# Performance work log

Hardware: AMD Instinct MI355X
Metric: run time of the kernel (lower is better)

The kernel has to match this reference:

```python
import jax, jax.numpy as jnp
import numpy as np

N, E, ET = 50000, 400000, 50000
F, ED, H, L = 64, 32, 128, 2


def _forward(x, edge_attr, target_edge_attr, node_W, node_b, edge_W, edge_b,
             pre_W, pre_b, post_W, post_b, lin_W, lin_b, bn_g, bn_b,
             em1_W, em1_b, em2_W, em2_b, edge_index):
    n = x.shape[0]
    h = node_W.shape[1]
    src, dst = edge_index[0], edge_index[1]
    x = x @ node_W + node_b                      # [N,H]
    ea = edge_attr @ edge_W + edge_b             # [E,H]
    tea = target_edge_attr @ edge_W + edge_b     # [Et,H]

    ones = jnp.ones((src.shape[0],), jnp.float32)
    cnt = jax.ops.segment_sum(ones, dst, num_segments=n)        # in-degree per node
    avg_deg_log = jnp.mean(jnp.log(cnt + 1.0))                  # PyG avg_deg['log'] from deg histogram
    deg = jnp.clip(cnt, 1.0)[:, None]
    amp = jnp.log(deg + 1.0) / avg_deg_log                      # 'amplification' scaler
    att = avg_deg_log / jnp.log(deg + 1.0)                      # 'attenuation' scaler
    cnt_c = jnp.clip(cnt, 1.0)[:, None]
    has = (cnt > 0)[:, None]

    nlayers = pre_W.shape[0]
    for i in range(nlayers):
        # pre-MLP on message cat([x_i(dst), x_j(src), edge_attr]); split matmul avoids [E,3H] concat
        Wd, Ws, We = pre_W[i, :h], pre_W[i, h:2 * h], pre_W[i, 2 * h:]
        m = x[dst] @ Wd + x[src] @ Ws + ea @ We + pre_b[i]      # [E,H]
        s = jax.ops.segment_sum(m, dst, num_segments=n)
        mean = s / cnt_c
        mean2 = jax.ops.segment_sum(m * m, dst, num_segments=n) / cnt_c
        std = jnp.sqrt(jax.nn.relu(mean2 - mean * mean) + 1e-5)  # PyG StdAggregation
        mn = jnp.where(has, jax.ops.segment_min(m, dst, num_segments=n), 0.0)
        mx = jnp.where(has, jax.ops.segment_max(m, dst, num_segments=n), 0.0)
        agg = jnp.concatenate([mean, mn, mx, std], axis=-1)     # [N,4H] aggregator order
        scaled = jnp.concatenate([agg, agg * amp, agg * att], axis=-1)  # [N,12H] scaler order
        # post-MLP on cat([x, scaled]); split matmul
        out = x @ post_W[i, :h] + scaled @ post_W[i, h:] + post_b[i]
        out = out @ lin_W[i] + lin_b[i]
        # BatchNorm (training mode, biased var, eps=1e-5)
        mu = out.mean(axis=0)
        var = jnp.mean((out - mu) ** 2, axis=0)
        bn = bn_g[i] * (out - mu) / jnp.sqrt(var + 1e-5) + bn_b[i]
        x = (x + jax.nn.relu(bn)) / 2
        # edge update: ea + MLP(cat([x[src], x[dst], ea])) / 2
        W1s, W1d, W1e = em1_W[i, :h], em1_W[i, h:2 * h], em1_W[i, 2 * h:]
        hid = jax.nn.relu(x[src] @ W1s + x[dst] @ W1d + ea @ W1e + em1_b[i])
        ea = ea + (hid @ em2_W[i] + em2_b[i]) / 2
    return (x, ea, tea)


def setup_inputs() -> dict:
    key = jax.random.key(0)
    ks = jax.random.split(key, 24)

    def w(k, shape):
        fan_in = shape[-2]
        return (jax.random.normal(k, shape, jnp.float32) / np.sqrt(fan_in)).astype(jnp.float32)

    inp = {
        'x': jax.random.normal(ks[0], (N, F), jnp.float32),
        'edge_attr': jax.random.normal(ks[1], (E, ED), jnp.float32),
        'target_edge_attr': jax.random.normal(ks[2], (ET, ED), jnp.float32),
        'node_W': w(ks[3], (F, H)), 'node_b': jnp.zeros((H,), jnp.float32),
        'edge_W': w(ks[4], (ED, H)), 'edge_b': jnp.zeros((H,), jnp.float32),
        'pre_W': w(ks[5], (L, 3 * H, H)), 'pre_b': jnp.zeros((L, H), jnp.float32),
        'post_W': w(ks[6], (L, 13 * H, H)), 'post_b': jnp.zeros((L, H), jnp.float32),
        'lin_W': w(ks[7], (L, H, H)), 'lin_b': jnp.zeros((L, H), jnp.float32),
        'bn_g': jnp.ones((L, H), jnp.float32), 'bn_b': jnp.zeros((L, H), jnp.float32),
        'em1_W': w(ks[8], (L, 3 * H, H)), 'em1_b': jnp.zeros((L, H), jnp.float32),
        'em2_W': w(ks[9], (L, H, H)), 'em2_b': jnp.zeros((L, H), jnp.float32),
        'edge_index': jax.random.randint(ks[10], (2, E), 0, N, dtype=jnp.int32),
    }
    return inp


def reference(x, edge_attr, target_edge_attr, node_W, node_b, edge_W, edge_b,
              pre_W, pre_b, post_W, post_b, lin_W, lin_b, bn_g, bn_b,
              em1_W, em1_b, em2_W, em2_b, edge_index):
    return _forward(x, edge_attr, target_edge_attr, node_W, node_b, edge_W, edge_b,
                    pre_W, pre_b, post_W, post_b, lin_W, lin_b, bn_g, bn_b,
                    em1_W, em1_b, em2_W, em2_b, edge_index)
```

## Files before the change

### kernel.cpp

```cpp
#include <hip/hip_runtime.h>
#include <math.h>

#define NN  50000
#define NE  400000
#define NTE 50000
#define FIN 64
#define EDIM 32
#define HD  128
#define NL  2
#define SCAN_B ((NN + 255) / 256)

typedef __attribute__((ext_vector_type(8))) short bf16x8;
typedef __attribute__((ext_vector_type(4))) short bf16x4;
typedef __attribute__((ext_vector_type(4))) float f32x4;

static __device__ __forceinline__ unsigned short f2bf(float f) {
    unsigned u = __float_as_uint(f);
    unsigned r = (u + 0x7fffu + ((u >> 16) & 1u)) >> 16;
    return (unsigned short)r;
}
static __device__ __forceinline__ float bfhi2f(unsigned u) { return __uint_as_float(u & 0xffff0000u); }
static __device__ __forceinline__ float bflo2f(unsigned u) { return __uint_as_float(u << 16); }

static __device__ __forceinline__ bf16x8 load_a8(const float* p, bool ok) {
    bf16x8 a = {};
    if (ok) {
        const float4 v0 = *(const float4*)(p);
        const float4 v1 = *(const float4*)(p + 4);
        a[0] = (short)f2bf(v0.x); a[1] = (short)f2bf(v0.y);
        a[2] = (short)f2bf(v0.z); a[3] = (short)f2bf(v0.w);
        a[4] = (short)f2bf(v1.x); a[5] = (short)f2bf(v1.y);
        a[6] = (short)f2bf(v1.z); a[7] = (short)f2bf(v1.w);
    }
    return a;
}
static __device__ __forceinline__ bf16x4 pack4(float4 a) {
    bf16x4 v;
    v[0]=(short)f2bf(a.x); v[1]=(short)f2bf(a.y); v[2]=(short)f2bf(a.z); v[3]=(short)f2bf(a.w);
    return v;
}

__global__ void __launch_bounds__(256) k_packW(const float* __restrict__ W,
        unsigned short* __restrict__ out, int K)
{
    const int tid = blockIdx.x * 256 + threadIdx.x;
    const int total = (K / 32) * 512;
    if (tid >= total) return;
    const int lane = tid & 63, nt = (tid >> 6) & 7, kb = tid >> 9;
    const int k0 = kb * 32 + (lane >> 4) * 8;
    const int col = nt * 16 + (lane & 15);
    bf16x8 v;
    #pragma unroll
    for (int j = 0; j < 8; ++j)
        v[j] = (short)f2bf(W[(size_t)(k0 + j) * HD + col]);
    *(bf16x8*)(out + (size_t)tid * 8) = v;
}

__global__ void __launch_bounds__(256) k_foldW(const float* __restrict__ edgeW,
        const float* __restrict__ edgeb, const float* __restrict__ We0,
        float* __restrict__ Wf, float* __restrict__ bf)
{
    const int tid = blockIdx.x * 256 + threadIdx.x;
    if (tid < 4096) {
        const int k = tid >> 7, c = tid & 127;
        float s = 0.f;
        for (int j = 0; j < 128; ++j) s += edgeW[k * HD + j] * We0[(size_t)j * HD + c];
        Wf[tid] = s;
    } else if (tid < 4224) {
        const int c = tid - 4096;
        float s = 0.f;
        for (int j = 0; j < 128; ++j) s += edgeb[j] * We0[(size_t)j * HD + c];
        bf[c] = s;
    }
}

template<int KB>
__global__ void __launch_bounds__(256) k_gemm_T(const float* A,
        const unsigned short* __restrict__ Wpk, const float* __restrict__ bias,
        float* C, int M)
{
    const int t = threadIdx.x, w = t >> 6, l = t & 63;
    const int n = blockIdx.x * 64 + w * 16 + (l & 15);
    const bool ok = n < M;
    const int q = l >> 4;
    const int K = KB * 32;
    f32x4 acc[8] = {};
    #pragma unroll
    for (int kb = 0; kb < KB; ++kb) {
        const bf16x8 b = load_a8(A + (size_t)n * K + kb * 32 + q * 8, ok);
        #pragma unroll
        for (int nt = 0; nt < 8; ++nt) {
            const bf16x8 aW = *(const bf16x8*)(Wpk + (((size_t)(kb * 8 + nt) * 64 + l) << 3));
            acc[nt] = __builtin_amdgcn_mfma_f32_16x16x32_bf16(aW, b, acc[nt], 0, 0, 0);
        }
    }
    if (ok) {
        float* pc = C + (size_t)n * HD + q * 4;
        #pragma unroll
        for (int nt = 0; nt < 8; ++nt) {
            const int col = nt * 16 + q * 4;
            float4 bv = bias ? *(const float4*)(bias + col) : make_float4(0.f,0.f,0.f,0.f);
            float4 o;
            o.x = acc[nt][0] + bv.x; o.y = acc[nt][1] + bv.y;
            o.z = acc[nt][2] + bv.z; o.w = acc[nt][3] + bv.w;
            *(float4*)(pc + nt * 16) = o;
        }
    }
}

template<int KB>
__global__ void __launch_bounds__(256) k_gemm2_Tb(const float* A,
        const unsigned short* __restrict__ W0, const unsigned short* __restrict__ W1,
        const float* __restrict__ b0, unsigned short* C0, unsigned short* C1, int M)
{
    const int t = threadIdx.x, w = t >> 6, l = t & 63;
    const int n = blockIdx.x * 64 + w * 16 + (l & 15);
    const bool ok = n < M;
    const int q = l >> 4;
    const int K = KB * 32;
    f32x4 a0[8] = {}, a1[8] = {};
    #pragma unroll
    for (int kb = 0; kb < KB; ++kb) {
        const bf16x8 b = load_a8(A + (size_t)n * K + kb * 32 + q * 8, ok);
        #pragma unroll
        for (int nt = 0; nt < 8; ++nt) {
            const bf16x8 u = *(const bf16x8*)(W0 + (((size_t)(kb * 8 + nt) * 64 + l) << 3));
            const bf16x8 v = *(const bf16x8*)(W1 + (((size_t)(kb * 8 + nt) * 64 + l) << 3));
            a0[nt] = __builtin_amdgcn_mfma_f32_16x16x32_bf16(u, b, a0[nt], 0, 0, 0);
            a1[nt] = __builtin_amdgcn_mfma_f32_16x16x32_bf16(v, b, a1[nt], 0, 0, 0);
        }
    }
    if (ok) {
        unsigned short* p0 = C0 + (size_t)n * HD + q * 4;
        unsigned short* p1 = C1 + (size_t)n * HD + q * 4;
        #pragma unroll
        for (int nt = 0; nt < 8; ++nt) {
            const int col = nt * 16 + q * 4;
            float4 bv = b0 ? *(const float4*)(b0 + col) : make_float4(0.f,0.f,0.f,0.f);
            float4 o0, o1;
            o0.x = a0[nt][0] + bv.x; o0.y = a0[nt][1] + bv.y;
            o0.z = a0[nt][2] + bv.z; o0.w = a0[nt][3] + bv.w;
            o1.x = a1[nt][0]; o1.y = a1[nt][1]; o1.z = a1[nt][2]; o1.w = a1[nt][3];
            *(bf16x4*)(p0 + nt * 16) = pack4(o0);
            *(bf16x4*)(p1 + nt * 16) = pack4(o1);
        }
    }
}

__global__ void __launch_bounds__(256) k_count(const int* __restrict__ d, int* __restrict__ cnt, int E)
{
    const int e = blockIdx.x * 256 + threadIdx.x;
    if (e < E) atomicAdd(&cnt[d[e]], 1);
}

__global__ void __launch_bounds__(256) k_avglog(const int* __restrict__ cnt, float* __restrict__ stats)
{
    float s = 0.f;
    for (int n = blockIdx.x * 256 + threadIdx.x; n < NN; n += gridDim.x * 256)
        s += logf((float)cnt[n] + 1.f);
    #pragma unroll
    for (int off = 32; off > 0; off >>= 1) s += __shfl_down(s, off);
    __shared__ float ls[4];
    if ((threadIdx.x & 63) == 0) ls[threadIdx.x >> 6] = s;
    __syncthreads();
    if (threadIdx.x == 0) unsafeAtomicAdd(stats, ls[0] + ls[1] + ls[2] + ls[3]);
}

__global__ void __launch_bounds__(256) k_scan_block(const int* __restrict__ cnt,
        int* __restrict__ incl, int* __restrict__ part)
{
    __shared__ int s[256];
    const int t = threadIdx.x;
    const int i = blockIdx.x * 256 + t;
    const int v = (i < NN) ? cnt[i] : 0;
    s[t] = v;
    __syncthreads();
    #pragma unroll
    for (int off = 1; off < 256; off <<= 1) {
        const int x = (t >= off) ? s[t - off] : 0;
        __syncthreads();
        s[t] += x;
        __syncthreads();
    }
    if (i < NN) incl[i] = s[t];
    if (t == 255) part[blockIdx.x] = s[255];
}

__global__ void __launch_bounds__(256) k_scan_part(const int* __restrict__ part,
        int* __restrict__ poff, int np)
{
    __shared__ int s[256];
    const int t = threadIdx.x;
    const int v = (t < np) ? part[t] : 0;
    s[t] = v;
    __syncthreads();
    #pragma unroll
    for (int off = 1; off < 256; off <<= 1) {
        const int x = (t >= off) ? s[t - off] : 0;
        __syncthreads();
        s[t] += x;
        __syncthreads();
    }
    poff[t] = s[t] - v;
}

__global__ void __launch_bounds__(256) k_scan_add(const int* __restrict__ incl,
        const int* __restrict__ cnt, const int* __restrict__ poff,
        int* __restrict__ row_start, int* __restrict__ cursor)
{
    const int i = blockIdx.x * 256 + threadIdx.x;
    if (i < NN) {
        const int excl = incl[i] - cnt[i] + poff[blockIdx.x];
        row_start[i] = excl;
        cursor[i] = excl;
    }
    if (i == 0) row_start[NN] = NE;
}

__global__ void __launch_bounds__(256) k_scatter(const int* __restrict__ dstp,
        int* cursor, int* __restrict__ sppos)
{
    const int e = blockIdx.x * 256 + threadIdx.x;
    if (e < NE) sppos[e] = atomicAdd(&cursor[dstp[e]], 1);
}

template<int KB>
__global__ void __launch_bounds__(256) k_msg_T(const float* __restrict__ EA,
        const unsigned short* __restrict__ Wpk, const float* __restrict__ bias,
        const unsigned short* __restrict__ xsb, const int* __restrict__ srcp,
        const int* __restrict__ sppos, unsigned short* __restrict__ mbuf)
{
    const int t = threadIdx.x, w = t >> 6, l = t & 63;
    const int e = blockIdx.x * 64 + w * 16 + (l & 15);
    const int q = l >> 4;
    f32x4 acc[8] = {};
    #pragma unroll
    for (int kb = 0; kb < KB; ++kb) {
        const bf16x8 bea = load_a8(EA + (size_t)e * (KB * 32) + kb * 32 + q * 8, true);
        #pragma unroll
        for (int nt = 0; nt < 8; ++nt) {
            const bf16x8 aW = *(const bf16x8*)(Wpk + (((size_t)(kb * 8 + nt) * 64 + l) << 3));
            acc[nt] = __builtin_amdgcn_mfma_f32_16x16x32_bf16(aW, bea, acc[nt], 0, 0, 0);
        }
    }
    const int sn = srcp[e], sp = sppos[e];
    const unsigned short* ps = xsb + (size_t)sn * HD + q * 4;
    unsigned short* pm = mbuf + (size_t)sp * HD + q * 4;
    #pragma unroll
    for (int nt = 0; nt < 8; ++nt) {
        const uint2 su = *(const uint2*)(ps + nt * 16);
        float4 o;
        o.x = acc[nt][0] + bflo2f(su.x); o.y = acc[nt][1] + bfhi2f(su.x);
        o.z = acc[nt][2] + bflo2f(su.y); o.w = acc[nt][3] + bfhi2f(su.y);
        if (bias) {
            const float4 bv = *(const float4*)(bias + nt * 16 + q * 4);
            o.x += bv.x; o.y += bv.y; o.z += bv.z; o.w += bv.w;
        }
        *(bf16x4*)(pm + nt * 16) = pack4(o);
    }
}

__global__ void __launch_bounds__(256) k_agg(const unsigned short* __restrict__ mbuf,
        const int* __restrict__ rs, const unsigned short* __restrict__ xdb,
        const float* __restrict__ stats, unsigned short* __restrict__ aggb)
{
    const int n = blockIdx.x * 4 + (threadIdx.x >> 6);
    if (n >= NN) return;
    const int lane = threadIdx.x & 63;
    const int c = lane * 2;
    const int s = rs[n], e = rs[n + 1];
    const unsigned xu = *(const unsigned*)(xdb + (size_t)n * HD + c);
    const float xv0 = bflo2f(xu), xv1 = bfhi2f(xu);
    float s0=0.f, s1=0.f, q0=0.f, q1=0.f;
    float mn0=INFINITY, mn1=INFINITY, mx0=-INFINITY, mx1=-INFINITY;
    for (int i = s; i < e; ++i) {
        const unsigned u = *(const unsigned*)(mbuf + (size_t)i * HD + c);
        const float v0 = bflo2f(u), v1 = bfhi2f(u);
        s0 += v0; s1 += v1;
        q0 += v0 * v0; q1 += v1 * v1;
        mn0 = fminf(mn0, v0); mn1 = fminf(mn1, v1);
        mx0 = fmaxf(mx0, v0); mx1 = fmaxf(mx1, v1);
    }
    const int deg = e - s;
    const float inv = 1.f / (float)(deg > 1 ? deg : 1);
    const float fd = (float)deg * inv;
    const float m0p = s0 * inv, m1p = s1 * inv;
    const float sd0 = sqrtf(fmaxf(q0 * inv - m0p * m0p, 0.f) + 1e-5f);
    const float sd1 = sqrtf(fmaxf(q1 * inv - m1p * m1p, 0.f) + 1e-5f);
    const bool has = deg > 0;
    const float v0[4] = { m0p + fd * xv0, has ? mn0 + xv0 : 0.f,
                          has ? mx0 + xv0 : 0.f, sd0 };
    const float v1[4] = { m1p + fd * xv1, has ? mn1 + xv1 : 0.f,
                          has ? mx1 + xv1 : 0.f, sd1 };
    const float avg = stats[0] * (1.f / (float)NN);
    const float lg = logf(fmaxf((float)deg, 1.f) + 1.f);
    const float amp = lg / avg, att = avg / lg;
    unsigned* a = (unsigned*)(aggb + (size_t)n * 1536 + c);
    #pragma unroll
    for (int sct = 0; sct < 4; ++sct) {
        a[sct * 64]       = (unsigned)f2bf(v0[sct])       | ((unsigned)f2bf(v1[sct]) << 16);
        a[256 + sct * 64] = (unsigned)f2bf(v0[sct] * amp) | ((unsigned)f2bf(v1[sct] * amp) << 16);
        a[512 + sct * 64] = (unsigned)f2bf(v0[sct] * att) | ((unsigned)f2bf(v1[sct] * att) << 16);
    }
}

__global__ void __launch_bounds__(256) k_post_lin_T(const float* __restrict__ x,
        const unsigned short* __restrict__ aggb, const unsigned short* __restrict__ PWpk,
        const float* __restrict__ pb, const unsigned short* __restrict__ LNpk,
        const float* __restrict__ lb, float* __restrict__ outb, int M)
{
    __shared__ unsigned short s_o16[64 * 128];
    const int t = threadIdx.x, w = t >> 6, l = t & 63;
    const int el = w * 16 + (l & 15);
    const int n = blockIdx.x * 64 + el;
    const bool ok = n < M;
    const int q = l >> 4;
    f32x4 acc[8] = {};
    #pragma unroll
    for (int kb = 0; kb < 4; ++kb) {
        const bf16x8 b = load_a8(x + (size_t)n * HD + kb * 32 + q * 8, ok);
        #pragma unroll
        for (int nt = 0; nt < 8; ++nt) {
            const bf16x8 aW = *(const bf16x8*)(PWpk + (((size_t)(kb * 8 + nt) * 64 + l) << 3));
            acc[nt] = __builtin_amdgcn_mfma_f32_16x16x32_bf16(aW, b, acc[nt], 0, 0, 0);
        }
    }
    const unsigned short* arow = aggb + (size_t)n * 1536 + q * 8;
    #pragma unroll 4
    for (int kb = 4; kb < 52; ++kb) {
        bf16x8 b = {};
        if (ok) b = *(const bf16x8*)(arow + (size_t)(kb - 4) * 32);
        #pragma unroll
        for (int nt = 0; nt < 8; ++nt) {
            const bf16x8 aW = *(const bf16x8*)(PWpk + (((size_t)(kb * 8 + nt) * 64 + l) << 3));
            acc[nt] = __builtin_amdgcn_mfma_f32_16x16x32_bf16(aW, b, acc[nt], 0, 0, 0);
        }
    }
    #pragma unroll
    for (int nt = 0; nt < 8; ++nt) {
        const int col = nt * 16 + q * 4;
        const float4 bv = *(const float4*)(pb + col);
        float4 o;
        o.x = acc[nt][0] + bv.x; o.y = acc[nt][1] + bv.y;
        o.z = acc[nt][2] + bv.z; o.w = acc[nt][3] + bv.w;
        const int bcol = nt * 32 + q * 8;
        const int slot = bcol >> 4;
        const int ba = el * 256 + ((slot ^ (el & 7)) << 4) + (bcol & 15);
        *(bf16x4*)((char*)s_o16 + ba) = pack4(o);
    }
    __syncthreads();
    f32x4 acc2[8] = {};
    #pragma unroll
    for (int kb = 0; kb < 4; ++kb) {
        const int slot = kb * 4 + q;
        const int ba = el * 256 + ((slot ^ (el & 7)) << 4);
        const bf16x8 bh = *(const bf16x8*)((const char*)s_o16 + ba);
        #pragma unroll
        for (int nt = 0; nt < 8; ++nt) {
            const bf16x8 aW = *(const bf16x8*)(LNpk + (((size_t)(kb * 8 + nt) * 64 + l) << 3));
            acc2[nt] = __builtin_amdgcn_mfma_f32_16x16x32_bf16(aW, bh, acc2[nt], 0, 0, 0);
        }
    }
    if (ok) {
        float* pc = outb + (size_t)n * HD + q * 4;
        #pragma unroll
        for (int nt = 0; nt < 8; ++nt) {
            const int col = nt * 16 + q * 4;
            const float4 bv = *(const float4*)(lb + col);
            float4 o;
            o.x = acc2[nt][0] + bv.x; o.y = acc2[nt][1] + bv.y;
            o.z = acc2[nt][2] + bv.z; o.w = acc2[nt][3] + bv.w;
            *(float4*)(pc + nt * 16) = o;
        }
    }
}

__global__ void __launch_bounds__(256) k_bnstats(const float* __restrict__ ob,
        float* __restrict__ bs, float* __restrict__ bq, int M)
{
    const int c = threadIdx.x & 127;
    const int gsub = threadIdx.x >> 7;
    float s = 0.f, qq = 0.f;
    for (int rr = blockIdx.x * 2 + gsub; rr < M; rr += gridDim.x * 2) {
        const float v = ob[(size_t)rr * HD + c];
        s += v; qq += v * v;
    }
    __shared__ float ls[2][HD], lq[2][HD];
    ls[gsub][c] = s; lq[gsub][c] = qq;
    __syncthreads();
    if (gsub == 0) {
        unsafeAtomicAdd(&bs[c], ls[0][c] + ls[1][c]);
        unsafeAtomicAdd(&bq[c], lq[0][c] + lq[1][c]);
    }
}

__global__ void __launch_bounds__(256) k_xupdate(float* x, const float* __restrict__ ob,
        const float* __restrict__ bs, const float* __restrict__ bq,
        const float* __restrict__ g, const float* __restrict__ bb)
{
    const int i = blockIdx.x * 256 + threadIdx.x;
    const int c0 = (i & 31) * 4;
    const float4 ov = ((const float4*)ob)[i];
    const float4 xv = ((const float4*)x)[i];
    const float o[4]  = {ov.x, ov.y, ov.z, ov.w};
    const float xo[4] = {xv.x, xv.y, xv.z, xv.w};
    float res[4];
    #pragma unroll
    for (int j = 0; j < 4; ++j) {
        const int c = c0 + j;
        const float mu  = bs[c] * (1.f / (float)NN);
        const float var = bq[c] * (1.f / (float)NN) - mu * mu;
        const float bn  = g[c] * (o[j] - mu) * rsqrtf(var + 1e-5f) + bb[c];
        res[j] = (xo[j] + fmaxf(bn, 0.f)) * 0.5f;
    }
    ((float4*)x)[i] = make_float4(res[0], res[1], res[2], res[3]);
}

__global__ void __launch_bounds__(256) k_edge_upd_T(float* ea,
        const unsigned short* __restrict__ W1epk, const unsigned short* __restrict__ e2pk,
        const float* __restrict__ e2b, const unsigned short* __restrict__ xs1b,
        const unsigned short* __restrict__ xd1b, const int* __restrict__ srcp,
        const int* __restrict__ dstp)
{
    __shared__ unsigned short s_hid[64 * 128];
    __shared__ float s_b2[128];
    const int t = threadIdx.x, w = t >> 6, l = t & 63;
    const int row0b = blockIdx.x * 64;
    if (t < 128) s_b2[t] = e2b[t];
    const int el = w * 16 + (l & 15);
    const int e = row0b + el;
    const int q = l >> 4, kq = q * 8;
    f32x4 acc1[8] = {};
    #pragma unroll
    for (int kb = 0; kb < 4; ++kb) {
        const bf16x8 bea = load_a8(ea + (size_t)e * HD + kb * 32 + kq, true);
        #pragma unroll
        for (int nt = 0; nt < 8; ++nt) {
            const bf16x8 aW = *(const bf16x8*)(W1epk + (((size_t)(kb * 8 + nt) * 64 + l) << 3));
            acc1[nt] = __builtin_amdgcn_mfma_f32_16x16x32_bf16(aW, bea, acc1[nt], 0, 0, 0);
        }
    }
    {
        const int sn = srcp[e], dn = dstp[e];
        const unsigned short* ps = xs1b + (size_t)sn * HD + q * 4;
        const unsigned short* pd = xd1b + (size_t)dn * HD + q * 4;
        #pragma unroll
        for (int nt = 0; nt < 8; ++nt) {
            const uint2 su = *(const uint2*)(ps + nt * 16);
            const uint2 du = *(const uint2*)(pd + nt * 16);
            float4 h;
            h.x = fmaxf(acc1[nt][0] + bflo2f(su.x) + bflo2f(du.x), 0.f);
            h.y = fmaxf(acc1[nt][1] + bfhi2f(su.x) + bfhi2f(du.x), 0.f);
            h.z = fmaxf(acc1[nt][2] + bflo2f(su.y) + bflo2f(du.y), 0.f);
            h.w = fmaxf(acc1[nt][3] + bfhi2f(su.y) + bfhi2f(du.y), 0.f);
            const int bcol = nt * 32 + q * 8;
            const int slot = bcol >> 4;
            const int ba = el * 256 + ((slot ^ (el & 7)) << 4) + (bcol & 15);
            *(bf16x4*)((char*)s_hid + ba) = pack4(h);
        }
    }
    __syncthreads();
    f32x4 acc2[8] = {};
    #pragma unroll
    for (int kb = 0; kb < 4; ++kb) {
        const int slot = kb * 4 + q;
        const int ba = el * 256 + ((slot ^ (el & 7)) << 4);
        const bf16x8 bh = *(const bf16x8*)((const char*)s_hid + ba);
        #pragma unroll
        for (int nt = 0; nt < 8; ++nt) {
            const bf16x8 aW = *(const bf16x8*)(e2pk + (((size_t)(kb * 8 + nt) * 64 + l) << 3));
            acc2[nt] = __builtin_amdgcn_mfma_f32_16x16x32_bf16(aW, bh, acc2[nt], 0, 0, 0);
        }
    }
    {
        float* pe = ea + (size_t)e * HD + q * 4;
        #pragma unroll
        for (int nt = 0; nt < 8; ++nt) {
            const float4 eo = *(const float4*)(pe + nt * 16);
            const float4 bv = *(const float4*)(&s_b2[nt * 16 + q * 4]);
            float4 o;
            o.x = eo.x + (acc2[nt][0] + bv.x) * 0.5f;
            o.y = eo.y + (acc2[nt][1] + bv.y) * 0.5f;
            o.z = eo.z + (acc2[nt][2] + bv.z) * 0.5f;
            o.w = eo.w + (acc2[nt][3] + bv.w) * 0.5f;
            *(float4*)(pe + nt * 16) = o;
        }
    }
}

extern "C" void kernel_launch(void* const* d_in, const int* in_sizes, int n_in,
                              void* d_out, int out_size, void* d_ws, size_t ws_size,
                              hipStream_t stream)
{
    const float* x0    = (const float*)d_in[0];
    const float* eatr  = (const float*)d_in[1];
    const float* teatr = (const float*)d_in[2];
    const float* nodeW = (const float*)d_in[3];
    const float* nodeb = (const float*)d_in[4];
    const float* edgeW = (const float*)d_in[5];
    const float* edgeb = (const float*)d_in[6];
    const float* preW  = (const float*)d_in[7];
    const float* preb  = (const float*)d_in[8];
    const float* postW = (const float*)d_in[9];
    const float* postb = (const float*)d_in[10];
    const float* linW  = (const float*)d_in[11];
    const float* linb  = (const float*)d_in[12];
    const float* bng   = (const float*)d_in[13];
    const float* bnb   = (const float*)d_in[14];
    const float* em1W  = (const float*)d_in[15];
    const float* em1b  = (const float*)d_in[16];
    const float* em2W  = (const float*)d_in[17];
    const float* em2b  = (const float*)d_in[18];
    const int*   eidx  = (const int*)d_in[19];
    const int* srcp = eidx;
    const int* dstp = eidx + NE;

    float* out_x  = (float*)d_out;
    float* out_ea = out_x + (size_t)NN * HD;
    float* out_te = out_ea + (size_t)NE * HD;

    const size_t NH = (size_t)NN * HD;
    const size_t EH = (size_t)NE * HD;
    unsigned short* xdb = (unsigned short*)d_ws;
    unsigned short* xsb = xdb + NH;
    float* outb  = (float*)(xsb + NH);
    float* stats = outb + NH;
    float* Wf    = stats + 512;
    float* bfold = Wf + 4096;
    int*   cnt      = (int*)(bfold + 128);
    int*   row_start = cnt + NN;
    int*   cursor   = row_start + NN + 1;
    int*   tmpincl  = cursor + NN;
    int*   part     = tmpincl + NN;
    int*   poff     = part + 256;
    int*   sppos    = poff + 256;
    unsigned short* mbuf = (unsigned short*)(((uintptr_t)(sppos + NE) + 15) & ~(uintptr_t)15);
    unsigned short* aggb = mbuf + EH;
    unsigned short* pk   = aggb + (size_t)NN * 1536;
    const size_t KBSZ = 512 * 8;
    unsigned short* pkPost = pk;
    unsigned short* pkPre  = pkPost + 104 * KBSZ;
    unsigned short* pkEm1  = pkPre  + 24 * KBSZ;
    unsigned short* pkLin  = pkEm1  + 24 * KBSZ;
    unsigned short* pkEm2  = pkLin  + 8 * KBSZ;
    unsigned short* pkNode = pkEm2  + 8 * KBSZ;
    unsigned short* pkEdge = pkNode + 2 * KBSZ;
    unsigned short* pkWe0f = pkEdge + 1 * KBSZ;

    hipMemsetAsync(cnt, 0, NN * sizeof(int), stream);
    hipMemsetAsync(stats, 0, 512 * sizeof(float), stream);

    k_packW<<<208, 256, 0, stream>>>(postW, pkPost, 3328);
    k_packW<<<48, 256, 0, stream>>>(preW,  pkPre,  768);
    k_packW<<<48, 256, 0, stream>>>(em1W,  pkEm1,  768);
    k_packW<<<16, 256, 0, stream>>>(linW,  pkLin,  256);
    k_packW<<<16, 256, 0, stream>>>(em2W,  pkEm2,  256);
    k_packW<<<4, 256, 0, stream>>>(nodeW, pkNode, 64);
    k_packW<<<2, 256, 0, stream>>>(edgeW, pkEdge, 32);
    k_foldW<<<17, 256, 0, stream>>>(edgeW, edgeb, preW + 256 * HD, Wf, bfold);
    k_packW<<<2, 256, 0, stream>>>(Wf, pkWe0f, 32);

    k_gemm_T<1><<<(NE + 63) / 64, 256, 0, stream>>>(eatr, pkEdge, edgeb, out_ea, NE);
    k_gemm_T<1><<<(NTE + 63) / 64, 256, 0, stream>>>(teatr, pkEdge, edgeb, out_te, NTE);
    k_gemm_T<2><<<(NN + 63) / 64, 256, 0, stream>>>(x0, pkNode, nodeb, out_x, NN);

    k_count<<<(NE + 255) / 256, 256, 0, stream>>>(dstp, cnt, NE);
    k_avglog<<<256, 256, 0, stream>>>(cnt, stats);
    k_scan_block<<<SCAN_B, 256, 0, stream>>>(cnt, tmpincl, part);
    k_scan_part<<<1, 256, 0, stream>>>(part, poff, SCAN_B);
    k_scan_add<<<SCAN_B, 256, 0, stream>>>(tmpincl, cnt, poff, row_start, cursor);
    k_scatter<<<(NE + 255) / 256, 256, 0, stream>>>(dstp, cursor, sppos);

    const int gn = (NN + 63) / 64;
    const int ge = NE / 64;

    for (int l = 0; l < NL; ++l) {
        const unsigned short* Wd_pk  = pkPre + (size_t)(l * 12 + 0) * KBSZ;
        const unsigned short* Ws_pk  = pkPre + (size_t)(l * 12 + 4) * KBSZ;
        const unsigned short* We_pk  = pkPre + (size_t)(l * 12 + 8) * KBSZ;
        const unsigned short* W1s_pk = pkEm1 + (size_t)(l * 12 + 0) * KBSZ;
        const unsigned short* W1d_pk = pkEm1 + (size_t)(l * 12 + 4) * KBSZ;
        const unsigned short* W1e_pk = pkEm1 + (size_t)(l * 12 + 8) * KBSZ;
        const unsigned short* PW_pk  = pkPost + (size_t)l * 52 * KBSZ;
        const unsigned short* lin_pk = pkLin + (size_t)l * 4 * KBSZ;
        const unsigned short* em2_pk = pkEm2 + (size_t)l * 4 * KBSZ;
        const float* pbl = preb + l * HD;
        const float* pob = postb + l * HD;
        const float* lb  = linb + l * HD;
        const float* g_  = bng + l * HD;
        const float* b_  = bnb + l * HD;
        const float* e1b = em1b + l * HD;
        const float* e2b = em2b + l * HD;

        hipMemsetAsync(stats + 128, 0, 256 * sizeof(float), stream);

        k_gemm2_Tb<4><<<gn, 256, 0, stream>>>(out_x, Wd_pk, Ws_pk, pbl, xdb, xsb, NN);
        if (l == 0)
            k_msg_T<1><<<ge, 256, 0, stream>>>(eatr, pkWe0f, bfold, xsb, srcp, sppos, mbuf);
        else
            k_msg_T<4><<<ge, 256, 0, stream>>>(out_ea, We_pk, nullptr, xsb, srcp, sppos, mbuf);
        k_agg<<<(NN + 3) / 4, 256, 0, stream>>>(mbuf, row_start, xdb, stats, aggb);
        k_post_lin_T<<<gn, 256, 0, stream>>>(out_x, aggb, PW_pk, pob, lin_pk, lb, outb, NN);
        k_bnstats<<<256, 256, 0, stream>>>(outb, stats + 128, stats + 256, NN);
        k_xupdate<<<NN * 32 / 256, 256, 0, stream>>>(out_x, outb, stats + 128, stats + 256, g_, b_);
        k_gemm2_Tb<4><<<gn, 256, 0, stream>>>(out_x, W1d_pk, W1s_pk, e1b, xdb, xsb, NN);
        k_edge_upd_T<<<ge, 256, 0, stream>>>(out_ea, W1e_pk, em2_pk, e2b, xsb, xdb, srcp, dstp);
    }
}
```

Before: 1.404 ms.

## Fuse layer-0 edge update with layer-1 message computation in one edge kernel

Layer 0's edge-update MLP and layer 1's pre-MLP message GEMM are merged into a single per-edge kernel. The updated edge features are staged in shared memory as bf16 and fed straight into the next message GEMM, so the separate k_msg_T pass no longer re-reads out_ea from global memory. This needs separate workspace buffers for the em1 node projections (xd1b/xs1b) and the layer-1 pre projections, plus an extra node GEMM launch before the fused kernel. The cost is higher shared memory per block and more register pressure, which may lower occupancy.

```diff
diff --git a/kernel.cpp b/kernel.cpp
--- a/kernel.cpp
+++ b/kernel.cpp
@@ -484,6 +484,111 @@
             o.z = eo.z + (acc2[nt][2] + bv.z) * 0.5f;
             o.w = eo.w + (acc2[nt][3] + bv.w) * 0.5f;
             *(float4*)(pe + nt * 16) = o;
+        }
+    }
+}
+
+__global__ void __launch_bounds__(256) k_edge_msg_fused(float* ea,
+        const unsigned short* __restrict__ W1epk, const unsigned short* __restrict__ e2pk,
+        const float* __restrict__ e2b,
+        const unsigned short* __restrict__ xs1b, const unsigned short* __restrict__ xd1b,
+        const unsigned short* __restrict__ WeNpk, const unsigned short* __restrict__ xsNb,
+        const int* __restrict__ srcp, const int* __restrict__ dstp,
+        const int* __restrict__ sppos, unsigned short* __restrict__ mbuf)
+{
+    __shared__ unsigned short s_hid[64 * 128];
+    __shared__ unsigned short s_ea1[64 * 128];
+    __shared__ float s_b2[128];
+    const int t = threadIdx.x, w = t >> 6, l = t & 63;
+    const int row0b = blockIdx.x * 64;
+    if (t < 128) s_b2[t] = e2b[t];
+    const int el = w * 16 + (l & 15);
+    const int e = row0b + el;
+    const int q = l >> 4, kq = q * 8;
+    const int sn = srcp[e], dn = dstp[e];
+    f32x4 acc1[8] = {};
+    #pragma unroll
+    for (int kb = 0; kb < 4; ++kb) {
+        const bf16x8 bea = load_a8(ea + (size_t)e * HD + kb * 32 + kq, true);
+        #pragma unroll
+        for (int nt = 0; nt < 8; ++nt) {
+            const bf16x8 aW = *(const bf16x8*)(W1epk + (((size_t)(kb * 8 + nt) * 64 + l) << 3));
+            acc1[nt] = __builtin_amdgcn_mfma_f32_16x16x32_bf16(aW, bea, acc1[nt], 0, 0, 0);
+        }
+    }
+    {
+        const unsigned short* ps = xs1b + (size_t)sn * HD + q * 4;
+        const unsigned short* pd = xd1b + (size_t)dn * HD + q * 4;
+        #pragma unroll
+        for (int nt = 0; nt < 8; ++nt) {
+            const uint2 su = *(const uint2*)(ps + nt * 16);
+            const uint2 du = *(const uint2*)(pd + nt * 16);
+            float4 h;
+            h.x = fmaxf(acc1[nt][0] + bflo2f(su.x) + bflo2f(du.x), 0.f);
+            h.y = fmaxf(acc1[nt][1] + bfhi2f(su.x) + bfhi2f(du.x), 0.f);
+            h.z = fmaxf(acc1[nt][2] + bflo2f(su.y) + bflo2f(du.y), 0.f);
+            h.w = fmaxf(acc1[nt][3] + bfhi2f(su.y) + bfhi2f(du.y), 0.f);
+            const int bcol = nt * 32 + q * 8;
+            const int slot = bcol >> 4;
+            const int ba = el * 256 + ((slot ^ (el & 7)) << 4) + (bcol & 15);
+            *(bf16x4*)((char*)s_hid + ba) = pack4(h);
+        }
+    }
+    __syncthreads();
+    f32x4 acc2[8] = {};
+    #pragma unroll
+    for (int kb = 0; kb < 4; ++kb) {
+        const int slot = kb * 4 + q;
+        const int ba = el * 256 + ((slot ^ (el & 7)) << 4);
+        const bf16x8 bh = *(const bf16x8*)((const char*)s_hid + ba);
+        #pragma unroll
+        for (int nt = 0; nt < 8; ++nt) {
+            const bf16x8 aW = *(const bf16x8*)(e2pk + (((size_t)(kb * 8 + nt) * 64 + l) << 3));
+            acc2[nt] = __builtin_amdgcn_mfma_f32_16x16x32_bf16(aW, bh, acc2[nt], 0, 0, 0);
+        }
+    }
+    {
+        float* pe = ea + (size_t)e * HD + q * 4;
+        #pragma unroll
+        for (int nt = 0; nt < 8; ++nt) {
+            const float4 eo = *(const float4*)(pe + nt * 16);
+            const float4 bv = *(const float4*)(&s_b2[nt * 16 + q * 4]);
+            float4 o;
+            o.x = eo.x + (acc2[nt][0] + bv.x) * 0.5f;
+            o.y = eo.y + (acc2[nt][1] + bv.y) * 0.5f;
+            o.z = eo.z + (acc2[nt][2] + bv.z) * 0.5f;
+            o.w = eo.w + (acc2[nt][3] + bv.w) * 0.5f;
+            *(float4*)(pe + nt * 16) = o;
+            const int bcol = nt * 32 + q * 8;
+            const int slot = bcol >> 4;
+            const int ba = el * 256 + ((slot ^ (el & 7)) << 4) + (bcol & 15);
+            *(bf16x4*)((char*)s_ea1 + ba) = pack4(o);
+        }
+    }
+    __syncthreads();
+    f32x4 acc3[8] = {};
+    #pragma unroll
+    for (int kb = 0; kb < 4; ++kb) {
+        const int slot = kb * 4 + q;
+        const int ba = el * 256 + ((slot ^ (el & 7)) << 4);
+        const bf16x8 be = *(const bf16x8*)((const char*)s_ea1 + ba);
+        #pragma unroll
+        for (int nt = 0; nt < 8; ++nt) {
+            const bf16x8 aW = *(const bf16x8*)(WeNpk + (((size_t)(kb * 8 + nt) * 64 + l) << 3));
+            acc3[nt] = __builtin_amdgcn_mfma_f32_16x16x32_bf16(aW, be, acc3[nt], 0, 0, 0);
+        }
+    }
+    {
+        const int sp = sppos[e];
+        const unsigned short* ps = xsNb + (size_t)sn * HD + q * 4;
+        unsigned short* pm = mbuf + (size_t)sp * HD + q * 4;
+        #pragma unroll
+        for (int nt = 0; nt < 8; ++nt) {
+            const uint2 su = *(const uint2*)(ps + nt * 16);
+            float4 o;
+            o.x = acc3[nt][0] + bflo2f(su.x); o.y = acc3[nt][1] + bfhi2f(su.x);
+            o.z = acc3[nt][2] + bflo2f(su.y); o.w = acc3[nt][3] + bfhi2f(su.y);
+            *(bf16x4*)(pm + nt * 16) = pack4(o);
         }
     }
 }
@@ -521,9 +626,11 @@
 
     const size_t NH = (size_t)NN * HD;
     const size_t EH = (size_t)NE * HD;
-    unsigned short* xdb = (unsigned short*)d_ws;
-    unsigned short* xsb = xdb + NH;
-    float* outb  = (float*)(xsb + NH);
+    unsigned short* xdb  = (unsigned short*)d_ws;
+    unsigned short* xsb  = xdb + NH;
+    unsigned short* xd1b = xsb + NH;
+    unsigned short* xs1b = xd1b + NH;
+    float* outb  = (float*)(xs1b + NH);
     float* stats = outb + NH;
     float* Wf    = stats + 512;
     float* bfold = Wf + 4096;
@@ -574,36 +681,37 @@
     const int gn = (NN + 63) / 64;
     const int ge = NE / 64;
 
+    const unsigned short *Wd_pk[NL], *Ws_pk[NL], *We_pk[NL];
+    const unsigned short *W1s_pk[NL], *W1d_pk[NL], *W1e_pk[NL];
+    const unsigned short *PW_pk[NL], *lin_pk[NL], *em2_pk[NL];
     for (int l = 0; l < NL; ++l) {
-        const unsigned short* Wd_pk  = pkPre + (size_t)(l * 12 + 0) * KBSZ;
-        const unsigned short* Ws_pk  = pkPre + (size_t)(l * 12 + 4) * KBSZ;
-        const unsigned short* We_pk  = pkPre + (size_t)(l * 12 + 8) * KBSZ;
-        const unsigned short* W1s_pk = pkEm1 + (size_t)(l * 12 + 0) * KBSZ;
-        const unsigned short* W1d_pk = pkEm1 + (size_t)(l * 12 + 4) * KBSZ;
-        const unsigned short* W1e_pk = pkEm1 + (size_t)(l * 12 + 8) * KBSZ;
-        const unsigned short* PW_pk  = pkPost + (size_t)l * 52 * KBSZ;
-        const unsigned short* lin_pk = pkLin + (size_t)l * 4 * KBSZ;
-        const unsigned short* em2_pk = pkEm2 + (size_t)l * 4 * KBSZ;
-        const float* pbl = preb + l * HD;
-        const float* pob = postb + l * HD;
-        const float* lb  = linb + l * HD;
-        const float* g_  = bng + l * HD;
-        const float* b_  = bnb + l * HD;
-        const float* e1b = em1b + l * HD;
-        const float* e2b = em2b + l * HD;
-
-        hipMemsetAsync(stats + 128, 0, 256 * sizeof(float), stream);
-
-        k_gemm2_Tb<4><<<gn, 256, 0, stream>>>(out_x, Wd_pk, Ws_pk, pbl, xdb, xsb, NN);
-        if (l == 0)
-            k_msg_T<1><<<ge, 256, 0, stream>>>(eatr, pkWe0f, bfold, xsb, srcp, sppos, mbuf);
-        else
-            k_msg_T<4><<<ge, 256, 0, stream>>>(out_ea, We_pk, nullptr, xsb, srcp, sppos, mbuf);
-        k_agg<<<(NN + 3) / 4, 256, 0, stream>>>(mbuf, row_start, xdb, stats, aggb);
-        k_post_lin_T<<<gn, 256, 0, stream>>>(out_x, aggb, PW_pk, pob, lin_pk, lb, outb, NN);
-        k_bnstats<<<256, 256, 0, stream>>>(outb, stats + 128, stats + 256, NN);
-        k_xupdate<<<NN * 32 / 256, 256, 0, stream>>>(out_x, outb, stats + 128, stats + 256, g_, b_);
-        k_gemm2_Tb<4><<<gn, 256, 0, stream>>>(out_x, W1d_pk, W1s_pk, e1b, xdb, xsb, NN);
-        k_edge_upd_T<<<ge, 256, 0, stream>>>(out_ea, W1e_pk, em2_pk, e2b, xsb, xdb, srcp, dstp);
-    }
-}
+        Wd_pk[l]  = pkPre + (size_t)(l * 12 + 0) * KBSZ;
+        Ws_pk[l]  = pkPre + (size_t)(l * 12 + 4) * KBSZ;
+        We_pk[l]  = pkPre + (size_t)(l * 12 + 8) * KBSZ;
+        W1s_pk[l] = pkEm1 + (size_t)(l * 12 + 0) * KBSZ;
+        W1d_pk[l] = pkEm1 + (size_t)(l * 12 + 4) * KBSZ;
+        W1e_pk[l] = pkEm1 + (size_t)(l * 12 + 8) * KBSZ;
+        PW_pk[l]  = pkPost + (size_t)l * 52 * KBSZ;
+        lin_pk[l] = pkLin + (size_t)l * 4 * KBSZ;
+        em2_pk[l] = pkEm2 + (size_t)l * 4 * KBSZ;
+    }
+
+    hipMemsetAsync(stats + 128, 0, 256 * sizeof(float), stream);
+    k_gemm2_Tb<4><<<gn, 256, 0, stream>>>(out_x, Wd_pk[0], Ws_pk[0], preb, xdb, xsb, NN);
+    k_msg_T<1><<<ge, 256, 0, stream>>>(eatr, pkWe0f, bfold, xsb, srcp, sppos, mbuf);
+    k_agg<<<(NN + 3) / 4, 256, 0, stream>>>(mbuf, row_start, xdb, stats, aggb);
+    k_post_lin_T<<<gn, 256, 0, stream>>>(out_x, aggb, PW_pk[0], postb, lin_pk[0], linb, outb, NN);
+    k_bnstats<<<256, 256, 0, stream>>>(outb, stats + 128, stats + 256, NN);
+    k_xupdate<<<NN * 32 / 256, 256, 0, stream>>>(out_x, outb, stats + 128, stats + 256, bng, bnb);
+    k_gemm2_Tb<4><<<gn, 256, 0, stream>>>(out_x, W1d_pk[0], W1s_pk[0], em1b, xd1b, xs1b, NN);
+    k_gemm2_Tb<4><<<gn, 256, 0, stream>>>(out_x, Wd_pk[1], Ws_pk[1], preb + HD, xdb, xsb, NN);
+    k_edge_msg_fused<<<ge, 256, 0, stream>>>(out_ea, W1e_pk[0], em2_pk[0], em2b,
+                                             xs1b, xd1b, We_pk[1], xsb, srcp, dstp, sppos, mbuf);
+    hipMemsetAsync(stats + 128, 0, 256 * sizeof(float), stream);
+    k_agg<<<(NN + 3) / 4, 256, 0, stream>>>(mbuf, row_start, xdb, stats, aggb);
+    k_post_lin_T<<<gn, 256, 0, stream>>>(out_x, aggb, PW_pk[1], postb + HD, lin_pk[1], linb + HD, outb, NN);
+    k_bnstats<<<256, 256, 0, stream>>>(outb, stats + 128, stats + 256, NN);
+    k_xupdate<<<NN * 32 / 256, 256, 0, stream>>>(out_x, outb, stats + 128, stats + 256, bng + HD, bnb + HD);
+    k_gemm2_Tb<4><<<gn, 256, 0, stream>>>(out_x, W1d_pk[1], W1s_pk[1], em1b + HD, xd1b, xs1b, NN);
+    k_edge_upd_T<<<ge, 256, 0, stream>>>(out_ea, W1e_pk[1], em2_pk[1], em2b + HD, xs1b, xd1b, srcp, dstp);
+}
```

New measurement: 1.464 ms. 4.2% more time.

## Permute node/message bf16 column layout to enable 16-byte stores and gathers

Applied to the files above, without the earlier changes.

Stores the bf16 node projections and per-edge messages in a permuted column order so each lane's two MFMA output tiles are contiguous, turning eight 8-byte stores and gathers into four 16-byte ones. The aggregation kernel and edge-MLP kernel index with the matching permutation. This aims to cut memory instructions and improve coalescing on the gather-heavy edge paths, at the cost of a non-standard layout that every consumer must agree on.

```diff
diff --git a/kernel.cpp b/kernel.cpp
--- a/kernel.cpp
+++ b/kernel.cpp
@@ -39,6 +39,13 @@
     v[0]=(short)f2bf(a.x); v[1]=(short)f2bf(a.y); v[2]=(short)f2bf(a.z); v[3]=(short)f2bf(a.w);
     return v;
 }
+static __device__ __forceinline__ bf16x8 pack8(float4 a, float4 b) {
+    bf16x8 v;
+    v[0]=(short)f2bf(a.x); v[1]=(short)f2bf(a.y); v[2]=(short)f2bf(a.z); v[3]=(short)f2bf(a.w);
+    v[4]=(short)f2bf(b.x); v[5]=(short)f2bf(b.y); v[6]=(short)f2bf(b.z); v[7]=(short)f2bf(b.w);
+    return v;
+}
+
 
 __global__ void __launch_bounds__(256) k_packW(const float* __restrict__ W,
         unsigned short* __restrict__ out, int K)
@@ -131,18 +138,20 @@
         }
     }
     if (ok) {
-        unsigned short* p0 = C0 + (size_t)n * HD + q * 4;
-        unsigned short* p1 = C1 + (size_t)n * HD + q * 4;
-        #pragma unroll
-        for (int nt = 0; nt < 8; ++nt) {
-            const int col = nt * 16 + q * 4;
-            float4 bv = b0 ? *(const float4*)(b0 + col) : make_float4(0.f,0.f,0.f,0.f);
-            float4 o0, o1;
-            o0.x = a0[nt][0] + bv.x; o0.y = a0[nt][1] + bv.y;
-            o0.z = a0[nt][2] + bv.z; o0.w = a0[nt][3] + bv.w;
-            o1.x = a1[nt][0]; o1.y = a1[nt][1]; o1.z = a1[nt][2]; o1.w = a1[nt][3];
-            *(bf16x4*)(p0 + nt * 16) = pack4(o0);
-            *(bf16x4*)(p1 + nt * 16) = pack4(o1);
+        unsigned short* p0 = C0 + (size_t)n * HD + q * 32;
+        unsigned short* p1 = C1 + (size_t)n * HD + q * 32;
+        #pragma unroll
+        for (int k = 0; k < 4; ++k) {
+            const int ntA = 2 * k, ntB = 2 * k + 1;
+            float4 bA = b0 ? *(const float4*)(b0 + ntA * 16 + q * 4) : make_float4(0.f,0.f,0.f,0.f);
+            float4 bB = b0 ? *(const float4*)(b0 + ntB * 16 + q * 4) : make_float4(0.f,0.f,0.f,0.f);
+            float4 oA, oB;
+            oA.x = a0[ntA][0]+bA.x; oA.y = a0[ntA][1]+bA.y; oA.z = a0[ntA][2]+bA.z; oA.w = a0[ntA][3]+bA.w;
+            oB.x = a0[ntB][0]+bB.x; oB.y = a0[ntB][1]+bB.y; oB.z = a0[ntB][2]+bB.z; oB.w = a0[ntB][3]+bB.w;
+            *(bf16x8*)(p0 + k * 8) = pack8(oA, oB);
+            float4 uA = make_float4(a1[ntA][0], a1[ntA][1], a1[ntA][2], a1[ntA][3]);
+            float4 uB = make_float4(a1[ntB][0], a1[ntB][1], a1[ntB][2], a1[ntB][3]);
+            *(bf16x8*)(p1 + k * 8) = pack8(uA, uB);
         }
     }
 }
@@ -244,19 +253,24 @@
         }
     }
     const int sn = srcp[e], sp = sppos[e];
-    const unsigned short* ps = xsb + (size_t)sn * HD + q * 4;
-    unsigned short* pm = mbuf + (size_t)sp * HD + q * 4;
-    #pragma unroll
-    for (int nt = 0; nt < 8; ++nt) {
-        const uint2 su = *(const uint2*)(ps + nt * 16);
-        float4 o;
-        o.x = acc[nt][0] + bflo2f(su.x); o.y = acc[nt][1] + bfhi2f(su.x);
-        o.z = acc[nt][2] + bflo2f(su.y); o.w = acc[nt][3] + bfhi2f(su.y);
+    const unsigned short* ps = xsb + (size_t)sn * HD + q * 32;
+    unsigned short* pm = mbuf + (size_t)sp * HD + q * 32;
+    #pragma unroll
+    for (int k = 0; k < 4; ++k) {
+        const int ntA = 2 * k, ntB = 2 * k + 1;
+        const uint4 su = *(const uint4*)(ps + k * 8);
+        float4 oA, oB;
+        oA.x = acc[ntA][0] + bflo2f(su.x); oA.y = acc[ntA][1] + bfhi2f(su.x);
+        oA.z = acc[ntA][2] + bflo2f(su.y); oA.w = acc[ntA][3] + bfhi2f(su.y);
+        oB.x = acc[ntB][0] + bflo2f(su.z); oB.y = acc[ntB][1] + bfhi2f(su.z);
+        oB.z = acc[ntB][2] + bflo2f(su.w); oB.w = acc[ntB][3] + bfhi2f(su.w);
         if (bias) {
-            const float4 bv = *(const float4*)(bias + nt * 16 + q * 4);
-            o.x += bv.x; o.y += bv.y; o.z += bv.z; o.w += bv.w;
-        }
-        *(bf16x4*)(pm + nt * 16) = pack4(o);
+            const float4 bA = *(const float4*)(bias + ntA * 16 + q * 4);
+            const float4 bB = *(const float4*)(bias + ntB * 16 + q * 4);
+            oA.x += bA.x; oA.y += bA.y; oA.z += bA.z; oA.w += bA.w;
+            oB.x += bB.x; oB.y += bB.y; oB.z += bB.z; oB.w += bB.w;
+        }
+        *(bf16x8*)(pm + k * 8) = pack8(oA, oB);
     }
 }
 
@@ -268,13 +282,14 @@
     if (n >= NN) return;
     const int lane = threadIdx.x & 63;
     const int c = lane * 2;
+    const int pidx = ((c & 12) << 3) + ((c >> 4) << 2) + (c & 3);
     const int s = rs[n], e = rs[n + 1];
-    const unsigned xu = *(const unsigned*)(xdb + (size_t)n * HD + c);
+    const unsigned xu = *(const unsigned*)(xdb + (size_t)n * HD + pidx);
     const float xv0 = bflo2f(xu), xv1 = bfhi2f(xu);
     float s0=0.f, s1=0.f, q0=0.f, q1=0.f;
     float mn0=INFINITY, mn1=INFINITY, mx0=-INFINITY, mx1=-INFINITY;
     for (int i = s; i < e; ++i) {
-        const unsigned u = *(const unsigned*)(mbuf + (size_t)i * HD + c);
+        const unsigned u = *(const unsigned*)(mbuf + (size_t)i * HD + pidx);
         const float v0 = bflo2f(u), v1 = bfhi2f(u);
         s0 += v0; s1 += v1;
         q0 += v0 * v0; q1 += v1 * v1;
@@ -442,21 +457,28 @@
     }
     {
         const int sn = srcp[e], dn = dstp[e];
-        const unsigned short* ps = xs1b + (size_t)sn * HD + q * 4;
-        const unsigned short* pd = xd1b + (size_t)dn * HD + q * 4;
-        #pragma unroll
-        for (int nt = 0; nt < 8; ++nt) {
-            const uint2 su = *(const uint2*)(ps + nt * 16);
-            const uint2 du = *(const uint2*)(pd + nt * 16);
-            float4 h;
-            h.x = fmaxf(acc1[nt][0] + bflo2f(su.x) + bflo2f(du.x), 0.f);
-            h.y = fmaxf(acc1[nt][1] + bfhi2f(su.x) + bfhi2f(du.x), 0.f);
-            h.z = fmaxf(acc1[nt][2] + bflo2f(su.y) + bflo2f(du.y), 0.f);
-            h.w = fmaxf(acc1[nt][3] + bfhi2f(su.y) + bfhi2f(du.y), 0.f);
-            const int bcol = nt * 32 + q * 8;
-            const int slot = bcol >> 4;
-            const int ba = el * 256 + ((slot ^ (el & 7)) << 4) + (bcol & 15);
-            *(bf16x4*)((char*)s_hid + ba) = pack4(h);
+        const unsigned short* ps = xs1b + (size_t)sn * HD + q * 32;
+        const unsigned short* pd = xd1b + (size_t)dn * HD + q * 32;
+        #pragma unroll
+        for (int k = 0; k < 4; ++k) {
+            const int ntA = 2 * k, ntB = 2 * k + 1;
+            const uint4 su = *(const uint4*)(ps + k * 8);
+            const uint4 du = *(const uint4*)(pd + k * 8);
+            float4 hA, hB;
+            hA.x = fmaxf(acc1[ntA][0] + bflo2f(su.x) + bflo2f(du.x), 0.f);
+            hA.y = fmaxf(acc1[ntA][1] + bfhi2f(su.x) + bfhi2f(du.x), 0.f);
+            hA.z = fmaxf(acc1[ntA][2] + bflo2f(su.y) + bflo2f(du.y), 0.f);
+            hA.w = fmaxf(acc1[ntA][3] + bfhi2f(su.y) + bfhi2f(du.y), 0.f);
+            hB.x = fmaxf(acc1[ntB][0] + bflo2f(su.z) + bflo2f(du.z), 0.f);
+            hB.y = fmaxf(acc1[ntB][1] + bfhi2f(su.z) + bfhi2f(du.z), 0.f);
+            hB.z = fmaxf(acc1[ntB][2] + bflo2f(su.w) + bflo2f(du.w), 0.f);
+            hB.w = fmaxf(acc1[ntB][3] + bfhi2f(su.w) + bfhi2f(du.w), 0.f);
+            const int bcolA = ntA * 32 + q * 8;
+            const int baA = el * 256 + (((bcolA >> 4) ^ (el & 7)) << 4) + (bcolA & 15);
+            *(bf16x4*)((char*)s_hid + baA) = pack4(hA);
+            const int bcolB = ntB * 32 + q * 8;
+            const int baB = el * 256 + (((bcolB >> 4) ^ (el & 7)) << 4) + (bcolB & 15);
+            *(bf16x4*)((char*)s_hid + baB) = pack4(hB);
         }
     }
     __syncthreads();
```

Result: slower. 1.438 ms (+2.4%).
